# Optimization experiments

Measured on AMD Instinct MI355X. Metric: run time of the kernel, lower is better.

## Reference

```python
import jax, jax.numpy as jnp
import numpy as np

N_NODES = 20000
N_EDGES = 320000
IN_FEATS = 64
HIDDENS = [128, 128, 128]
K = 4        # n_kernels
DIM = 2      # pseudo_coord


def setup_inputs() -> dict:
    key = jax.random.key(0)
    ks = jax.random.split(key, 32)
    inp = {
        "features": jax.random.normal(ks[0], (N_NODES, IN_FEATS), dtype=jnp.float32),
        "pseudo": jax.random.uniform(ks[1], (N_EDGES, DIM), dtype=jnp.float32),
        "src": jax.random.randint(ks[2], (N_EDGES,), 0, N_NODES, dtype=jnp.int32),
        "dst": jax.random.randint(ks[3], (N_EDGES,), 0, N_NODES, dtype=jnp.int32),
    }
    dims_in = [IN_FEATS] + HIDDENS[:-1]
    ki = 4
    for i, (din, dout) in enumerate(zip(dims_in, HIDDENS)):
        inp[f"fc_w{i}"] = jax.random.normal(ks[ki], (din, K * dout), dtype=jnp.float32) * (1.0 / np.sqrt(din)); ki += 1
        inp[f"mu{i}"] = jax.random.normal(ks[ki], (K, DIM), dtype=jnp.float32) * 0.1; ki += 1
        inp[f"inv_sigma{i}"] = jnp.ones((K, DIM), dtype=jnp.float32)
        inp[f"bias{i}"] = jnp.zeros((dout,), dtype=jnp.float32)
        inp[f"pw{i}"] = jax.random.normal(ks[ki], (DIM, DIM), dtype=jnp.float32) * 0.5; ki += 1
        inp[f"pb{i}"] = jnp.zeros((DIM,), dtype=jnp.float32)
    return inp


def _gmm_layer(h, pseudo, src, dst, fc_w, mu, inv_sigma, bias, pw, pb):
    k, dim = mu.shape
    dout = fc_w.shape[1] // k
    hp = (h @ fc_w).reshape(-1, k, dout)              # [N, K, out]
    u = jnp.tanh(pseudo @ pw + pb)                    # [E, dim] per-layer pseudo projection
    diff = (u[:, None, :] - mu[None, :, :]) * inv_sigma[None, :, :]
    w = jnp.exp(-0.5 * jnp.sum(diff * diff, axis=-1))  # [E, K] Gaussian mixture weights
    msg = jnp.einsum('ek,eko->eo', w, hp[src])         # gather + weighted mix -> [E, out]
    agg = jax.ops.segment_sum(msg, dst, num_segments=h.shape[0])  # scatter-sum
    return agg + bias


def reference(features, pseudo, src, dst,
              fc_w0, mu0, inv_sigma0, bias0, pw0, pb0,
              fc_w1, mu1, inv_sigma1, bias1, pw1, pb1,
              fc_w2, mu2, inv_sigma2, bias2, pw2, pb2):
    h = features
    h = _gmm_layer(h, pseudo, src, dst, fc_w0, mu0, inv_sigma0, bias0, pw0, pb0)
    h = _gmm_layer(h, pseudo, src, dst, fc_w1, mu1, inv_sigma1, bias1, pw1, pb1)
    h = _gmm_layer(h, pseudo, src, dst, fc_w2, mu2, inv_sigma2, bias2, pw2, pb2)
    return h
```

## Files before the change

kernel.cpp:

```cpp
#include <hip/hip_runtime.h>
#include <hip/hip_bf16.h>
#include <hip/hip_fp16.h>
#include <math.h>

#define NN 20000
#define NE 320000
#define SLOT 64

typedef __attribute__((ext_vector_type(8))) _Float16 f16x8;
typedef __attribute__((ext_vector_type(2))) _Float16 h16x2;
typedef __attribute__((ext_vector_type(4))) float f32x4;

__device__ inline ushort f2h(float f) {
    __half h = __float2half_rn(f);
    return *reinterpret_cast<ushort*>(&h);
}
__device__ inline uint pack2h(float a, float b) {
    return (uint)f2h(a) | ((uint)f2h(b) << 16);
}
__device__ inline h16x2 u2h2(uint x) {
    union { uint u; h16x2 h; } c; c.u = x; return c.h;
}
__device__ inline uint pack_lo(uint x, uint y) {
    return __builtin_amdgcn_perm(x, y, 0x01000504u);
}
__device__ inline uint pack_hi(uint x, uint y) {
    return __builtin_amdgcn_perm(x, y, 0x03020706u);
}

__device__ inline float fast_tanh(float x) {
    x = fminf(fmaxf(x, -9.f), 9.f);
    float e = __expf(2.f * x);
    return 1.f - 2.f / (e + 1.f);
}

struct EdgeParams {
    const float *pw0, *pb0, *mu0, *is0;
    const float *pw1, *pb1, *mu1, *is1;
    const float *pw2, *pb2, *mu2, *is2;
};

__device__ inline void layer_w(float p0, float p1, const float* pw, const float* pb,
                               const float* mu, const float* is, float* out4) {
    float u0 = fast_tanh(p0 * pw[0] + p1 * pw[2] + pb[0]);
    float u1 = fast_tanh(p0 * pw[1] + p1 * pw[3] + pb[1]);
#pragma unroll
    for (int k = 0; k < 4; ++k) {
        float d0 = (u0 - mu[k * 2 + 0]) * is[k * 2 + 0];
        float d1 = (u1 - mu[k * 2 + 1]) * is[k * 2 + 1];
        out4[k] = __expf(-0.5f * (d0 * d0 + d1 * d1));
    }
}

__global__ void fill_prep(const int* __restrict__ dst, const int* __restrict__ src,
                          const float* __restrict__ pseudo, EdgeParams P,
                          int* __restrict__ cursor, uint* __restrict__ recs,
                          const float* __restrict__ features, ushort* __restrict__ fbf,
                          const float* __restrict__ f0, const float* __restrict__ f1,
                          const float* __restrict__ f2, ushort* __restrict__ w0,
                          ushort* __restrict__ w1, ushort* __restrict__ w2) {
    __shared__ float tile[64][65];
    int bid = blockIdx.x;
    if (bid < 1250) {
        int e = bid * 256 + threadIdx.x;
        int n = dst[e];
        int pos = atomicAdd(&cursor[n], 1);
        if (pos < SLOT) {
            size_t slot = (size_t)n * SLOT + pos;
            float2 p = *(const float2*)(pseudo + (size_t)e * 2);
            float w[4];
            uint pk0x, pk0y, pk1x, pk1y, pk2x, pk2y;
            layer_w(p.x, p.y, P.pw0, P.pb0, P.mu0, P.is0, w);
            pk0x = pack2h(w[0], w[1]);
            pk0y = pack2h(w[2], w[3]);
            layer_w(p.x, p.y, P.pw1, P.pb1, P.mu1, P.is1, w);
            pk1x = pack2h(w[0], w[1]);
            pk1y = pack2h(w[2], w[3]);
            layer_w(p.x, p.y, P.pw2, P.pb2, P.mu2, P.is2, w);
            pk2x = pack2h(w[0], w[1]);
            pk2y = pack2h(w[2], w[3]);
            uint* r = recs + slot * 8;
            *(uint4*)(r + 0) = make_uint4((uint)src[e], 0u, pk0x, pk0y);
            *(uint4*)(r + 4) = make_uint4(pk1x, pk1y, pk2x, pk2y);
        }
    } else if (bid < 1290) {
        int b = bid - 1250;
        const float* srcp;
        ushort* dstp;
        int din, KD, k, nt, dt;
        if (b < 8)       { srcp = f0; dstp = w0; din = 64;  KD = 256; k = b >> 1; nt = b & 1; dt = 0; }
        else if (b < 24) { int t = b - 8;  srcp = f1; dstp = w1; din = 128; KD = 512; k = t >> 2; nt = (t >> 1) & 1; dt = t & 1; }
        else             { int t = b - 24; srcp = f2; dstp = w2; din = 128; KD = 512; k = t >> 2; nt = (t >> 1) & 1; dt = t & 1; }
        int n0 = nt * 64, d0 = dt * 64;
        int tx = threadIdx.x & 63, ty = threadIdx.x >> 6;
#pragma unroll
        for (int ii = 0; ii < 16; ++ii) {
            int dr = ty * 16 + ii;
            tile[dr][tx] = srcp[(size_t)(d0 + dr) * 512 + k * 128 + n0 + tx];
        }
        __syncthreads();
#pragma unroll
        for (int ii = 0; ii < 16; ++ii) {
            int nr = ty * 16 + ii;
            dstp[(size_t)(n0 + nr) * KD + k * din + d0 + tx] = f2h(tile[tx][nr]);
        }
    } else {
        int idx = (bid - 1290) * 256 + threadIdx.x;
        size_t b8 = (size_t)idx * 8;
        float4 a = *(const float4*)(features + b8);
        float4 b = *(const float4*)(features + b8 + 4);
        uint4 o;
        o.x = pack2h(a.x, a.y);
        o.y = pack2h(a.z, a.w);
        o.z = pack2h(b.x, b.y);
        o.w = pack2h(b.z, b.w);
        *(uint4*)(fbf + b8) = o;
    }
}

template <int DIN, bool OUTF16>
__global__ __launch_bounds__(1024, 8) void layer_fused(
    const ushort* __restrict__ hbf, const int* __restrict__ cursor,
    const uint* __restrict__ recs, int woff,
    const ushort* __restrict__ Bt, const float* __restrict__ bias,
    void* __restrict__ hout) {
    constexpr int KD = 4 * DIN;
    constexpr int PITCH = KD + 8;
    constexpr int B = 8;
    constexpr int FPL = DIN / 32;
    __shared__ __align__(16) ushort Ts[16 * PITCH];
    __shared__ __align__(16) f32x4 red[8][64];
    int wv = threadIdx.x >> 6, lane = threadIdx.x & 63;
    int l16 = lane & 15, quad = lane >> 4;
    int half = lane >> 5, l32 = lane & 31;
    int nb = blockIdx.x * 16;
    int n = nb + wv;

    {
        int deg = __builtin_amdgcn_readfirstlane(cursor[n]);
        deg = deg < SLOT ? deg : SLOT;
        size_t base = (size_t)n * SLOT;

        float acc[4 * FPL];
#pragma unroll
        for (int j = 0; j < 4 * FPL; ++j) acc[j] = 0.f;

        for (int i = 0; i < deg; i += 2 * B) {
            int s[B];
            uint wlo[B], whi[B];
            uint2 hv[B];
#pragma unroll
            for (int u = 0; u < B; ++u) {
                int ii = i + 2 * u + half;
                bool ok = ii < deg;
                size_t idx = base + (ok ? ii : 0);
                const uint* r = recs + idx * 8;
                s[u] = (int)r[0];
                uint2 wp = *(const uint2*)(r + woff);
                wlo[u] = ok ? wp.x : 0u;
                whi[u] = ok ? wp.y : 0u;
            }
#pragma unroll
            for (int u = 0; u < B; ++u) {
                const ushort* rowp = hbf + (size_t)s[u] * DIN + l32 * FPL;
                if (DIN == 64)
                    hv[u].x = *(const uint*)rowp;
                else
                    hv[u] = *(const uint2*)rowp;
            }
#pragma unroll
            for (int u = 0; u < B; u += 2) {
                uint wp0 = pack_lo(wlo[u], wlo[u + 1]);
                uint wp1 = pack_hi(wlo[u], wlo[u + 1]);
                uint wp2 = pack_lo(whi[u], whi[u + 1]);
                uint wp3 = pack_hi(whi[u], whi[u + 1]);
                h16x2 w2[4] = {u2h2(wp0), u2h2(wp1), u2h2(wp2), u2h2(wp3)};
                h16x2 f2[FPL];
                f2[0] = u2h2(pack_lo(hv[u].x, hv[u + 1].x));
                f2[1] = u2h2(pack_hi(hv[u].x, hv[u + 1].x));
                if (DIN == 128) {
                    f2[2] = u2h2(pack_lo(hv[u].y, hv[u + 1].y));
                    f2[3] = u2h2(pack_hi(hv[u].y, hv[u + 1].y));
                }
#pragma unroll
                for (int k = 0; k < 4; ++k)
#pragma unroll
                    for (int j = 0; j < FPL; ++j)
                        acc[k * FPL + j] = __builtin_amdgcn_fdot2(
                            w2[k], f2[j], acc[k * FPL + j], false);
            }
        }
#pragma unroll
        for (int j = 0; j < 4 * FPL; ++j) acc[j] += __shfl_xor(acc[j], 32);

        if (half == 0) {
#pragma unroll
            for (int k = 0; k < 4; ++k) {
                if (DIN == 64) {
                    ushort2 p;
                    p.x = f2h(acc[k * 2 + 0]);
                    p.y = f2h(acc[k * 2 + 1]);
                    *(ushort2*)(Ts + wv * PITCH + k * DIN + l32 * 2) = p;
                } else {
                    ushort4 p;
                    p.x = f2h(acc[k * 4 + 0]);
                    p.y = f2h(acc[k * 4 + 1]);
                    p.z = f2h(acc[k * 4 + 2]);
                    p.w = f2h(acc[k * 4 + 3]);
                    *(ushort4*)(Ts + wv * PITCH + k * DIN + l32 * 4) = p;
                }
            }
        }
    }
    __syncthreads();

    {
        constexpr int KH = KD / 2;
        int kh = wv >> 3;
        int ct = wv & 7;
        int c0 = ct * 16;
        f32x4 accg = (f32x4){0.f, 0.f, 0.f, 0.f};
        int kbeg = kh * KH;
#pragma unroll 4
        for (int k0 = kbeg; k0 < kbeg + KH; k0 += 32) {
            f16x8 af = *(const f16x8*)(Ts + l16 * PITCH + k0 + quad * 8);
            f16x8 bfr = *(const f16x8*)(Bt + (size_t)(c0 + l16) * KD + k0 + quad * 8);
            accg = __builtin_amdgcn_mfma_f32_16x16x32_f16(af, bfr, accg, 0, 0, 0);
        }
        if (kh == 1) red[ct][lane] = accg;
        __syncthreads();
        if (kh == 0) {
            f32x4 other = red[ct][lane];
            int gn = c0 + l16;
            float bv = bias[gn];
#pragma unroll
            for (int i = 0; i < 4; ++i) {
                int gm = nb + quad * 4 + i;
                float val = accg[i] + other[i] + bv;
                if (OUTF16)
                    ((ushort*)hout)[(size_t)gm * 128 + gn] = f2h(val);
                else
                    ((float*)hout)[(size_t)gm * 128 + gn] = val;
            }
        }
    }
}

extern "C" void kernel_launch(void* const* d_in, const int* in_sizes, int n_in,
                              void* d_out, int out_size, void* d_ws, size_t ws_size,
                              hipStream_t stream) {
    const float* features = (const float*)d_in[0];
    const float* pseudo = (const float*)d_in[1];
    const int* src = (const int*)d_in[2];
    const int* dst = (const int*)d_in[3];
    const float* fc_w[3] = {(const float*)d_in[4], (const float*)d_in[10], (const float*)d_in[16]};
    const float* mu[3] = {(const float*)d_in[5], (const float*)d_in[11], (const float*)d_in[17]};
    const float* isg[3] = {(const float*)d_in[6], (const float*)d_in[12], (const float*)d_in[18]};
    const float* bias[3] = {(const float*)d_in[7], (const float*)d_in[13], (const float*)d_in[19]};
    const float* pw[3] = {(const float*)d_in[8], (const float*)d_in[14], (const float*)d_in[20]};
    const float* pb[3] = {(const float*)d_in[9], (const float*)d_in[15], (const float*)d_in[21]};

    char* ws = (char*)d_ws;
    auto alloc = [&](size_t bytes) -> void* {
        void* p = (void*)ws;
        ws += (bytes + 255) & ~(size_t)255;
        return p;
    };
    int* cursor = (int*)alloc((size_t)NN * 4);
    uint* recs = (uint*)alloc((size_t)NN * SLOT * 32);
    ushort* fbf = (ushort*)alloc((size_t)NN * 64 * 2);
    ushort* w2t_0 = (ushort*)alloc((size_t)128 * 256 * 2);
    ushort* w2t_1 = (ushort*)alloc((size_t)128 * 512 * 2);
    ushort* w2t_2 = (ushort*)alloc((size_t)128 * 512 * 2);
    ushort* h1 = (ushort*)alloc((size_t)NN * 128 * 2);
    ushort* h2 = (ushort*)alloc((size_t)NN * 128 * 2);

    hipMemsetAsync(cursor, 0, (size_t)NN * 4, stream);
    EdgeParams P;
    P.pw0 = pw[0]; P.pb0 = pb[0]; P.mu0 = mu[0]; P.is0 = isg[0];
    P.pw1 = pw[1]; P.pb1 = pb[1]; P.mu1 = mu[1]; P.is1 = isg[1];
    P.pw2 = pw[2]; P.pb2 = pb[2]; P.mu2 = mu[2]; P.is2 = isg[2];
    fill_prep<<<1915, 256, 0, stream>>>(dst, src, pseudo, P, cursor, recs, features, fbf,
                                        fc_w[0], fc_w[1], fc_w[2], w2t_0, w2t_1, w2t_2);

    const int GB = NN / 16;

    layer_fused<64, true><<<GB, 1024, 0, stream>>>(
        fbf, cursor, recs, 2, w2t_0, bias[0], h1);
    layer_fused<128, true><<<GB, 1024, 0, stream>>>(
        h1, cursor, recs, 4, w2t_1, bias[1], h2);
    layer_fused<128, false><<<GB, 1024, 0, stream>>>(
        h2, cursor, recs, 6, w2t_2, bias[2], (float*)d_out);
}
```

Measured before the change: 229.9 us.

## Split edge scatter from Gaussian weight computation into separate per-layer arrays

The scatter kernel now writes only a compact (src, half-precision pseudo) record per slot, and a new dense kernel computes the three layers' mixture weights over all slots, writing them to separate per-layer arrays. Each layer kernel then reads the src array plus its own weight array instead of a 32-byte interleaved record. The intent is to shorten the atomic scatter path and cut the bytes each layer loads per edge. The cost is an extra launch, computing weights for every slot including empty ones (about four times the real edges), extra memory traffic, and rounding pseudo to fp16 before the tanh.

```diff
diff --git a/kernel.cpp b/kernel.cpp
--- a/kernel.cpp
+++ b/kernel.cpp
@@ -20,6 +20,10 @@
 }
 __device__ inline h16x2 u2h2(uint x) {
     union { uint u; h16x2 h; } c; c.u = x; return c.h;
+}
+__device__ inline float2 uh2f2(uint u) {
+    union { uint i; __half2 h; } c; c.i = u;
+    return __half22float2(c.h);
 }
 __device__ inline uint pack_lo(uint x, uint y) {
     return __builtin_amdgcn_perm(x, y, 0x01000504u);
@@ -52,9 +56,9 @@
     }
 }
 
-__global__ void fill_prep(const int* __restrict__ dst, const int* __restrict__ src,
-                          const float* __restrict__ pseudo, EdgeParams P,
-                          int* __restrict__ cursor, uint* __restrict__ recs,
+__global__ void k_scatter(const int* __restrict__ dst, const int* __restrict__ src,
+                          const float* __restrict__ pseudo,
+                          int* __restrict__ cursor, uint2* __restrict__ sp,
                           const float* __restrict__ features, ushort* __restrict__ fbf,
                           const float* __restrict__ f0, const float* __restrict__ f1,
                           const float* __restrict__ f2, ushort* __restrict__ w0,
@@ -66,22 +70,8 @@
         int n = dst[e];
         int pos = atomicAdd(&cursor[n], 1);
         if (pos < SLOT) {
-            size_t slot = (size_t)n * SLOT + pos;
             float2 p = *(const float2*)(pseudo + (size_t)e * 2);
-            float w[4];
-            uint pk0x, pk0y, pk1x, pk1y, pk2x, pk2y;
-            layer_w(p.x, p.y, P.pw0, P.pb0, P.mu0, P.is0, w);
-            pk0x = pack2h(w[0], w[1]);
-            pk0y = pack2h(w[2], w[3]);
-            layer_w(p.x, p.y, P.pw1, P.pb1, P.mu1, P.is1, w);
-            pk1x = pack2h(w[0], w[1]);
-            pk1y = pack2h(w[2], w[3]);
-            layer_w(p.x, p.y, P.pw2, P.pb2, P.mu2, P.is2, w);
-            pk2x = pack2h(w[0], w[1]);
-            pk2y = pack2h(w[2], w[3]);
-            uint* r = recs + slot * 8;
-            *(uint4*)(r + 0) = make_uint4((uint)src[e], 0u, pk0x, pk0y);
-            *(uint4*)(r + 4) = make_uint4(pk1x, pk1y, pk2x, pk2y);
+            sp[(size_t)n * SLOT + pos] = make_uint2((uint)src[e], pack2h(p.x, p.y));
         }
     } else if (bid < 1290) {
         int b = bid - 1250;
@@ -118,10 +108,24 @@
     }
 }
 
+__global__ void k_wcompute(const uint2* __restrict__ sp, EdgeParams P,
+                           uint2* __restrict__ cw0, uint2* __restrict__ cw1,
+                           uint2* __restrict__ cw2) {
+    int slot = blockIdx.x * 256 + threadIdx.x;
+    float2 p = uh2f2(sp[slot].y);
+    float w[4];
+    layer_w(p.x, p.y, P.pw0, P.pb0, P.mu0, P.is0, w);
+    cw0[slot] = make_uint2(pack2h(w[0], w[1]), pack2h(w[2], w[3]));
+    layer_w(p.x, p.y, P.pw1, P.pb1, P.mu1, P.is1, w);
+    cw1[slot] = make_uint2(pack2h(w[0], w[1]), pack2h(w[2], w[3]));
+    layer_w(p.x, p.y, P.pw2, P.pb2, P.mu2, P.is2, w);
+    cw2[slot] = make_uint2(pack2h(w[0], w[1]), pack2h(w[2], w[3]));
+}
+
 template <int DIN, bool OUTF16>
 __global__ __launch_bounds__(1024, 8) void layer_fused(
     const ushort* __restrict__ hbf, const int* __restrict__ cursor,
-    const uint* __restrict__ recs, int woff,
+    const uint2* __restrict__ sp, const uint2* __restrict__ cw,
     const ushort* __restrict__ Bt, const float* __restrict__ bias,
     void* __restrict__ hout) {
     constexpr int KD = 4 * DIN;
@@ -154,9 +158,8 @@
                 int ii = i + 2 * u + half;
                 bool ok = ii < deg;
                 size_t idx = base + (ok ? ii : 0);
-                const uint* r = recs + idx * 8;
-                s[u] = (int)r[0];
-                uint2 wp = *(const uint2*)(r + woff);
+                s[u] = (int)sp[idx].x;
+                uint2 wp = cw[idx];
                 wlo[u] = ok ? wp.x : 0u;
                 whi[u] = ok ? wp.y : 0u;
             }
@@ -267,7 +270,10 @@
         return p;
     };
     int* cursor = (int*)alloc((size_t)NN * 4);
-    uint* recs = (uint*)alloc((size_t)NN * SLOT * 32);
+    uint2* sp = (uint2*)alloc((size_t)NN * SLOT * 8);
+    uint2* cw0 = (uint2*)alloc((size_t)NN * SLOT * 8);
+    uint2* cw1 = (uint2*)alloc((size_t)NN * SLOT * 8);
+    uint2* cw2 = (uint2*)alloc((size_t)NN * SLOT * 8);
     ushort* fbf = (ushort*)alloc((size_t)NN * 64 * 2);
     ushort* w2t_0 = (ushort*)alloc((size_t)128 * 256 * 2);
     ushort* w2t_1 = (ushort*)alloc((size_t)128 * 512 * 2);
@@ -280,15 +286,17 @@
     P.pw0 = pw[0]; P.pb0 = pb[0]; P.mu0 = mu[0]; P.is0 = isg[0];
     P.pw1 = pw[1]; P.pb1 = pb[1]; P.mu1 = mu[1]; P.is1 = isg[1];
     P.pw2 = pw[2]; P.pb2 = pb[2]; P.mu2 = mu[2]; P.is2 = isg[2];
-    fill_prep<<<1915, 256, 0, stream>>>(dst, src, pseudo, P, cursor, recs, features, fbf,
+
+    k_scatter<<<1915, 256, 0, stream>>>(dst, src, pseudo, cursor, sp, features, fbf,
                                         fc_w[0], fc_w[1], fc_w[2], w2t_0, w2t_1, w2t_2);
+    k_wcompute<<<5000, 256, 0, stream>>>(sp, P, cw0, cw1, cw2);
 
     const int GB = NN / 16;
 
     layer_fused<64, true><<<GB, 1024, 0, stream>>>(
-        fbf, cursor, recs, 2, w2t_0, bias[0], h1);
+        fbf, cursor, sp, cw0, w2t_0, bias[0], h1);
     layer_fused<128, true><<<GB, 1024, 0, stream>>>(
-        h1, cursor, recs, 4, w2t_1, bias[1], h2);
+        h1, cursor, sp, cw1, w2t_1, bias[1], h2);
     layer_fused<128, false><<<GB, 1024, 0, stream>>>(
-        h2, cursor, recs, 6, w2t_2, bias[2], (float*)d_out);
-}
+        h2, cursor, sp, cw2, w2t_2, bias[2], (float*)d_out);
+}
```

After: 235.3 us. 1.02x slower.
